# Kernel tuning notes

Measured on AMD Instinct MI355X. Metric: run time of the kernel, lower is better.

Reference implementation:

```python
import jax, jax.numpy as jnp
import numpy as np

N_NODES = 20000
N_EDGES = 640000
NODE_NF = 64
HIDDEN = 256
N_LAYERS = 4


def _linear_init(key, fan_in, fan_out, layers=None):
    shape = (fan_in, fan_out) if layers is None else (layers, fan_in, fan_out)
    scale = 1.0 / np.sqrt(fan_in)
    return jax.random.normal(key, shape, dtype=jnp.float32) * scale


def setup_inputs() -> dict:
    key = jax.random.key(0)
    ks = jax.random.split(key, 16)
    L, H = N_LAYERS, HIDDEN
    return {
        "h": jax.random.normal(ks[0], (N_NODES, NODE_NF), dtype=jnp.float32),
        "edge_index": jax.random.randint(ks[1], (2, N_EDGES), 0, N_NODES, dtype=jnp.int64),
        "coord_diff": jax.random.normal(ks[2], (N_EDGES, 3), dtype=jnp.float32),
        # embedding in / out
        "w_in": _linear_init(ks[3], NODE_NF, H),
        "b_in": jnp.zeros((H,), jnp.float32),
        "w_out": _linear_init(ks[4], H, NODE_NF),
        "b_out": jnp.zeros((NODE_NF,), jnp.float32),
        # per-layer edge MLP: Linear(2H+1 -> H), silu, Linear(H -> H), silu
        "edge_w1": _linear_init(ks[5], 2 * H + 1, H, L),
        "edge_b1": jnp.zeros((L, H), jnp.float32),
        "edge_w2": _linear_init(ks[6], H, H, L),
        "edge_b2": jnp.zeros((L, H), jnp.float32),
        # per-layer node MLP: Linear(2H -> H), silu, Linear(H -> H)
        "node_w1": _linear_init(ks[7], 2 * H, H, L),
        "node_b1": jnp.zeros((L, H), jnp.float32),
        "node_w2": _linear_init(ks[8], H, H, L),
        "node_b2": jnp.zeros((L, H), jnp.float32),
    }


def reference(h, edge_index, coord_diff, w_in, b_in, w_out, b_out,
              edge_w1, edge_b1, edge_w2, edge_b2,
              node_w1, node_b1, node_w2, node_b2):
    row, col = edge_index[0], edge_index[1]
    # radial is layer-independent: [E, 1]
    radial = jnp.sum(coord_diff ** 2, axis=1, keepdims=True)

    h = h @ w_in + b_in  # [N, H]
    n_nodes = h.shape[0]

    for l in range(N_LAYERS):
        # edge model: gather endpoints, concat with radial, 2-layer MLP
        m = jnp.concatenate([h[row], h[col], radial], axis=1)  # [E, 2H+1]
        m = jax.nn.silu(m @ edge_w1[l] + edge_b1[l])
        m = jax.nn.silu(m @ edge_w2[l] + edge_b2[l])  # [E, H]
        # node model: segment-sum aggregate over row, concat, 2-layer MLP
        agg = jax.ops.segment_sum(m, row, num_segments=n_nodes)  # [N, H]
        x = jnp.concatenate([h, agg], axis=1)  # [N, 2H]
        x = jax.nn.silu(x @ node_w1[l] + node_b1[l])
        h = x @ node_w2[l] + node_b2[l]  # recurrent=False: no residual

    return h @ w_out + b_out  # [N, node_nf]
```

## Files before the change

kernel.cpp:

```cpp
#include <hip/hip_runtime.h>
#include <hip/hip_bf16.h>
#include <cstdint>
#include <cstddef>

#define NN 20000
#define NE 640000
#define NF 64
#define HD 256
#define NL 4
#define HTS 640

typedef __attribute__((ext_vector_type(8))) short short8;
typedef __attribute__((ext_vector_type(4))) float f32x4;
typedef __attribute__((ext_vector_type(2))) float f32x2;

__device__ __forceinline__ float bf2f(unsigned short u){
  union { unsigned int i; float f; } x; x.i = ((unsigned int)u) << 16; return x.f;
}
__device__ __forceinline__ unsigned short f2bf(float f){
  union { float f; unsigned int i; } x; x.f = f;
  unsigned int r = x.i + 0x7FFFu + ((x.i >> 16) & 1u);
  return (unsigned short)(r >> 16);
}
__device__ __forceinline__ unsigned int pk2bf(float a, float b){
  union { __hip_bfloat162 h; unsigned int u; } cv;
  cv.h = __float22bfloat162_rn(float2{a, b});
  return cv.u;
}
__device__ __forceinline__ float silu_f(float v){
  float e = __builtin_amdgcn_exp2f(v * -1.442695041f);
  return v * __builtin_amdgcn_rcpf(1.0f + e);
}
__device__ __forceinline__ f32x2 silu2(f32x2 v){
  f32x2 t = v * (f32x2){-1.442695041f, -1.442695041f};
  f32x2 e = (f32x2){__builtin_amdgcn_exp2f(t.x), __builtin_amdgcn_exp2f(t.y)};
  f32x2 d = e + (f32x2){1.0f, 1.0f};
  f32x2 r = (f32x2){__builtin_amdgcn_rcpf(d.x), __builtin_amdgcn_rcpf(d.y)};
  return v * r;
}
__device__ __forceinline__ void async16(const void* g, void* l){
  __builtin_amdgcn_global_load_lds(
      (const __attribute__((address_space(1))) unsigned int*)g,
      (__attribute__((address_space(3))) unsigned int*)l, 16, 0, 0);
}

__global__ __launch_bounds__(256) void prep_small(
    const float* __restrict__ w_in, const float* __restrict__ w_out,
    const float* __restrict__ ew1, const float* __restrict__ ew2,
    const float* __restrict__ nw1, const float* __restrict__ nw2,
    const float* __restrict__ eb1,
    unsigned short* __restrict__ w_in_t, unsigned short* __restrict__ w_out_t,
    unsigned short* __restrict__ ew1cat, float* __restrict__ w1r,
    float* __restrict__ b1e,
    unsigned short* __restrict__ ew2t, unsigned short* __restrict__ nw1t,
    unsigned short* __restrict__ nw2t)
{
  const int s = blockIdx.y;
  const int tid = blockIdx.x * 256 + threadIdx.x;
  if (s == 18) {
    if (tid < NL * 512) {
      int l = tid >> 9, c = tid & 511;
      b1e[tid] = (c < 256) ? eb1[l * HD + c] : 0.0f;
    }
    return;
  }
  if (s >= 2 && s < 6) {
    int l = s - 2;
    if (tid >= 513 * HD) return;
    int k = tid / HD, n = tid - k * HD;
    float v = ew1[(size_t)l * 513 * HD + tid];
    if (k == 512) { w1r[l * HD + n] = v; return; }
    unsigned short* dst = ew1cat + (size_t)l * 512 * 256;
    if (k < 256) dst[(size_t)n * 256 + k] = f2bf(v);
    else         dst[(size_t)(256 + n) * 256 + (k - 256)] = f2bf(v);
    return;
  }
  const float* src; unsigned short* dst; int K, N;
  if (s == 0)      { src = w_in;  dst = w_in_t;  K = NF;   N = HD; }
  else if (s == 1) { src = w_out; dst = w_out_t; K = HD;   N = NF; }
  else if (s < 10) { int l = s-6;  src = ew2 + (size_t)l*HD*HD;   dst = ew2t + (size_t)l*HD*HD;  K = HD;   N = HD; }
  else if (s < 14) { int l = s-10; src = nw1 + (size_t)l*2*HD*HD; dst = nw1t + (size_t)l*HD*512; K = 2*HD; N = HD; }
  else             { int l = s-14; src = nw2 + (size_t)l*HD*HD;   dst = nw2t + (size_t)l*HD*HD;  K = HD;   N = HD; }
  if (tid >= K * N) return;
  int k = tid / N, n = tid - k * N;
  dst[(size_t)n * K + k] = f2bf(src[tid]);
}

__global__ __launch_bounds__(256) void prep_big(
    const float* __restrict__ h_in, const float* __restrict__ cd,
    unsigned short* __restrict__ hb_in, float* __restrict__ radial)
{
  const int s = blockIdx.y;
  const int tid = blockIdx.x * 256 + threadIdx.x;
  if (s == 0) {
    if (tid < NN * NF) hb_in[tid] = f2bf(h_in[tid]);
  } else {
    if (tid < NE) {
      float x = cd[tid*3+0], y = cd[tid*3+1], z = cd[tid*3+2];
      radial[tid] = x*x + y*y + z*z;
    }
  }
}

__global__ __launch_bounds__(256) void hist_k(const int* __restrict__ erow, int* __restrict__ hist){
  int e = blockIdx.x * 256 + threadIdx.x;
  if (e < NE){
    unsigned r = (unsigned)erow[e]; if (r >= NN) r = 0;
    atomicAdd(&hist[r], 1);
  }
}

__global__ __launch_bounds__(256) void scan_k(const int* __restrict__ hist,
                                              int* __restrict__ starts, int* __restrict__ cursor){
  __shared__ int part[256];
  const int t = threadIdx.x;
  const int CH = 79;
  int lo = t * CH, hi = lo + CH; if (hi > NN) hi = NN; if (lo > NN) lo = NN;
  int s = 0;
  for (int i = lo; i < hi; ++i) s += hist[i];
  part[t] = s; __syncthreads();
  for (int off = 1; off < 256; off <<= 1){
    int v = (t >= off) ? part[t - off] : 0;
    __syncthreads();
    part[t] += v;
    __syncthreads();
  }
  int base = (t == 0) ? 0 : part[t - 1];
  for (int i = lo; i < hi; ++i){ starts[i] = base; cursor[i] = base; base += hist[i]; }
  if (t == 255) starts[NN] = part[255];
}

__global__ __launch_bounds__(256) void scatter_k(const int* __restrict__ erow,
                                                 const int* __restrict__ ecol,
                                                 const float* __restrict__ radial,
                                                 int* __restrict__ cursor,
                                                 int* __restrict__ rowcol,
                                                 float* __restrict__ radial_s){
  int e = blockIdx.x * 256 + threadIdx.x;
  if (e < NE){
    unsigned r = (unsigned)erow[e]; if (r >= NN) r = 0;
    unsigned c = (unsigned)ecol[e]; if (c >= NN) c = 0;
    int pos = atomicAdd(&cursor[r], 1);
    rowcol[2*pos]   = (int)r;
    rowcol[2*pos+1] = (int)c;
    radial_s[pos] = radial[e];
  }
}

__global__ __launch_bounds__(256, 4) void node0_k(
    const unsigned short* __restrict__ hb,
    const unsigned short* __restrict__ w_in_t,
    const float* __restrict__ b_in,
    const unsigned short* __restrict__ w1cat0,
    const float* __restrict__ b1e0,
    unsigned short* __restrict__ hcur,
    unsigned short* __restrict__ hT,
    int M)
{
  __shared__ __align__(16) unsigned short As[32*64];
  __shared__ __align__(16) unsigned short Bs[256*32];
  __shared__ __align__(16) unsigned short xL[8*32*32];
  const int t = threadIdx.x;
  const int lane = t & 63, wave = t >> 6;
  const int ln15 = lane & 15, q = lane >> 4;
  const int bm = blockIdx.x;
  const int sc = (t & 3) * 8;
  const int srB = t >> 2;

  float bvin[4];
  #pragma unroll
  for (int j = 0; j < 4; ++j) bvin[j] = b_in[wave*64 + j*16 + ln15];

  f32x4 acc[2][4];
  #pragma unroll
  for (int i = 0; i < 2; ++i)
    #pragma unroll
    for (int j = 0; j < 4; ++j) acc[i][j] = (f32x4){0.f,0.f,0.f,0.f};

  async16(hb + (size_t)(bm*32 + (t >> 3)) * NF + (t & 7)*8, &As[t*8]);

  for (int kt = 0; kt < 2; ++kt) {
    #pragma unroll
    for (int i = 0; i < 4; ++i)
      async16(w_in_t + (size_t)(i*64 + srB) * NF + kt*32 + sc, &Bs[i*2048 + t*8]);
    __syncthreads();
    short8 fa[2], fb[4];
    #pragma unroll
    for (int i = 0; i < 2; ++i) fa[i] = *(const short8*)&As[(i*16 + ln15)*64 + kt*32 + q*8];
    #pragma unroll
    for (int j = 0; j < 4; ++j) fb[j] = *(const short8*)&Bs[(wave*64 + j*16 + ln15)*32 + q*8];
    #pragma unroll
    for (int i = 0; i < 2; ++i)
      #pragma unroll
      for (int j = 0; j < 4; ++j)
        acc[i][j] = __builtin_amdgcn_mfma_f32_16x16x32_bf16(fa[i], fb[j], acc[i][j], 0, 0, 0);
    __syncthreads();
  }

  #pragma unroll
  for (int i = 0; i < 2; ++i) {
    #pragma unroll
    for (int j = 0; j < 4; ++j) {
      const int n = wave*64 + j*16 + ln15;
      const int kt2 = n >> 5, k31 = n & 31;
      const int r0 = i*16 + q*4;
      const int m0 = bm*32 + r0;
      #pragma unroll
      for (int r = 0; r < 4; ++r) {
        unsigned short h = f2bf(acc[i][j][r] + bvin[j]);
        hcur[(size_t)(m0 + r) * HD + n] = h;
        xL[kt2*1024 + (r0 + r)*32 + k31] = h;
      }
    }
  }

  #pragma unroll
  for (int half = 0; half < 2; ++half) {
    #pragma unroll
    for (int i = 0; i < 2; ++i)
      #pragma unroll
      for (int j = 0; j < 4; ++j) acc[i][j] = (f32x4){0.f,0.f,0.f,0.f};
    for (int kt2 = 0; kt2 < 8; ++kt2) {
      #pragma unroll
      for (int i = 0; i < 4; ++i)
        async16(w1cat0 + (size_t)(half*256 + i*64 + srB) * 256 + kt2*32 + sc,
                &Bs[i*2048 + t*8]);
      __syncthreads();
      short8 fa[2], fb[4];
      #pragma unroll
      for (int i = 0; i < 2; ++i) fa[i] = *(const short8*)&xL[kt2*1024 + (i*16 + ln15)*32 + q*8];
      #pragma unroll
      for (int j = 0; j < 4; ++j) fb[j] = *(const short8*)&Bs[(wave*64 + j*16 + ln15)*32 + q*8];
      #pragma unroll
      for (int i = 0; i < 2; ++i)
        #pragma unroll
        for (int j = 0; j < 4; ++j)
          acc[i][j] = __builtin_amdgcn_mfma_f32_16x16x32_bf16(fa[i], fb[j], acc[i][j], 0, 0, 0);
      __syncthreads();
    }
    #pragma unroll
    for (int i = 0; i < 2; ++i) {
      #pragma unroll
      for (int j = 0; j < 4; ++j) {
        const int n = half*256 + wave*64 + j*16 + ln15;
        const float bv = b1e0[n];
        #pragma unroll
        for (int r = 0; r < 4; ++r) {
          const int m = bm*32 + i*16 + q*4 + r;
          hT[(size_t)m * HTS + n] = f2bf(acc[i][j][r] + bv);
        }
      }
    }
  }
  (void)M;
}

__global__ __launch_bounds__(256, 4) void node_k(
    unsigned short* __restrict__ hcur,
    float* __restrict__ aggF,
    const unsigned short* __restrict__ w1t,
    const float* __restrict__ b1,
    const unsigned short* __restrict__ w2t,
    const float* __restrict__ b2,
    const unsigned short* __restrict__ w1cat_next,
    const float* __restrict__ b1e_next,
    unsigned short* __restrict__ hT,
    const unsigned short* __restrict__ w_out_t,
    const float* __restrict__ b_out,
    float* __restrict__ outF,
    int M)
{
  __shared__ __align__(16) unsigned short As[32*32];
  __shared__ __align__(16) unsigned short Bs[256*32];
  __shared__ __align__(16) unsigned short xL[8*32*32];
  const int t = threadIdx.x;
  const int lane = t & 63, wave = t >> 6;
  const int ln15 = lane & 15, q = lane >> 4;
  const int bm = blockIdx.x;
  const int sc = (t & 3) * 8;
  const int srA = (t & 127) >> 2;
  const int srB = t >> 2;

  const int rowA = bm*32 + srA;
  const unsigned short* aSrc = hcur + (size_t)rowA * HD + sc;
  float* gSrc = aggF + (size_t)rowA * HD + sc;

  float bv1[4], bv2[4];
  #pragma unroll
  for (int j = 0; j < 4; ++j) {
    bv1[j] = b1[wave*64 + j*16 + ln15];
    bv2[j] = b2[wave*64 + j*16 + ln15];
  }

  f32x4 acc[2][4];
  #pragma unroll
  for (int i = 0; i < 2; ++i)
    #pragma unroll
    for (int j = 0; j < 4; ++j) acc[i][j] = (f32x4){0.f,0.f,0.f,0.f};

  for (int kt = 0; kt < 16; ++kt) {
    if (t < 128) {
      if (kt < 8) {
        async16(aSrc + kt*32, &As[t*8]);
      } else {
        float* p = gSrc + (kt-8)*32;
        float4 a0 = *(const float4*)p;
        float4 a1 = *(const float4*)(p + 4);
        union { unsigned int u[4]; short8 s8; } cv;
        cv.u[0] = pk2bf(a0.x, a0.y); cv.u[1] = pk2bf(a0.z, a0.w);
        cv.u[2] = pk2bf(a1.x, a1.y); cv.u[3] = pk2bf(a1.z, a1.w);
        *(float4*)p = float4{0.f,0.f,0.f,0.f};
        *(float4*)(p + 4) = float4{0.f,0.f,0.f,0.f};
        *(short8*)&As[t*8] = cv.s8;
      }
    }
    #pragma unroll
    for (int i = 0; i < 4; ++i)
      async16(w1t + (size_t)(i*64 + srB) * 512 + kt*32 + sc, &Bs[i*2048 + t*8]);
    __syncthreads();
    short8 fa[2], fb[4];
    #pragma unroll
    for (int i = 0; i < 2; ++i) fa[i] = *(const short8*)&As[(i*16 + ln15)*32 + q*8];
    #pragma unroll
    for (int j = 0; j < 4; ++j) fb[j] = *(const short8*)&Bs[(wave*64 + j*16 + ln15)*32 + q*8];
    #pragma unroll
    for (int i = 0; i < 2; ++i)
      #pragma unroll
      for (int j = 0; j < 4; ++j)
        acc[i][j] = __builtin_amdgcn_mfma_f32_16x16x32_bf16(fa[i], fb[j], acc[i][j], 0, 0, 0);
    __syncthreads();
  }

  #pragma unroll
  for (int i = 0; i < 2; ++i) {
    #pragma unroll
    for (int j = 0; j < 4; ++j) {
      const int k = wave*64 + j*16 + ln15;
      const int kt2 = k >> 5, k31 = k & 31;
      const f32x2 bb = (f32x2){bv1[j], bv1[j]};
      f32x2 s01 = (f32x2){acc[i][j][0], acc[i][j][1]} + bb;
      f32x2 s23 = (f32x2){acc[i][j][2], acc[i][j][3]} + bb;
      f32x2 r01 = silu2(s01);
      f32x2 r23 = silu2(s23);
      const int r0 = i*16 + q*4;
      xL[kt2*1024 + (r0  )*32 + k31] = f2bf(r01.x);
      xL[kt2*1024 + (r0+1)*32 + k31] = f2bf(r01.y);
      xL[kt2*1024 + (r0+2)*32 + k31] = f2bf(r23.x);
      xL[kt2*1024 + (r0+3)*32 + k31] = f2bf(r23.y);
    }
  }
  #pragma unroll
  for (int i = 0; i < 2; ++i)
    #pragma unroll
    for (int j = 0; j < 4; ++j) acc[i][j] = (f32x4){0.f,0.f,0.f,0.f};

  for (int kt2 = 0; kt2 < 8; ++kt2) {
    #pragma unroll
    for (int i = 0; i < 4; ++i)
      async16(w2t + (size_t)(i*64 + srB) * 256 + kt2*32 + sc, &Bs[i*2048 + t*8]);
    __syncthreads();
    short8 fa[2], fb[4];
    #pragma unroll
    for (int i = 0; i < 2; ++i) fa[i] = *(const short8*)&xL[kt2*1024 + (i*16 + ln15)*32 + q*8];
    #pragma unroll
    for (int j = 0; j < 4; ++j) fb[j] = *(const short8*)&Bs[(wave*64 + j*16 + ln15)*32 + q*8];
    #pragma unroll
    for (int i = 0; i < 2; ++i)
      #pragma unroll
      for (int j = 0; j < 4; ++j)
        acc[i][j] = __builtin_amdgcn_mfma_f32_16x16x32_bf16(fa[i], fb[j], acc[i][j], 0, 0, 0);
    __syncthreads();
  }

  #pragma unroll
  for (int i = 0; i < 2; ++i) {
    #pragma unroll
    for (int j = 0; j < 4; ++j) {
      const int n = wave*64 + j*16 + ln15;
      const int kt2 = n >> 5, k31 = n & 31;
      const int r0 = i*16 + q*4;
      const int m0 = bm*32 + r0;
      #pragma unroll
      for (int r = 0; r < 4; ++r) {
        unsigned short h = f2bf(acc[i][j][r] + bv2[j]);
        hcur[(size_t)(m0 + r) * HD + n] = h;
        xL[kt2*1024 + (r0 + r)*32 + k31] = h;
      }
    }
  }

  if (w1cat_next) {
    #pragma unroll
    for (int half = 0; half < 2; ++half) {
      #pragma unroll
      for (int i = 0; i < 2; ++i)
        #pragma unroll
        for (int j = 0; j < 4; ++j) acc[i][j] = (f32x4){0.f,0.f,0.f,0.f};
      for (int kt2 = 0; kt2 < 8; ++kt2) {
        #pragma unroll
        for (int i = 0; i < 4; ++i)
          async16(w1cat_next + (size_t)(half*256 + i*64 + srB) * 256 + kt2*32 + sc,
                  &Bs[i*2048 + t*8]);
        __syncthreads();
        short8 fa[2], fb[4];
        #pragma unroll
        for (int i = 0; i < 2; ++i) fa[i] = *(const short8*)&xL[kt2*1024 + (i*16 + ln15)*32 + q*8];
        #pragma unroll
        for (int j = 0; j < 4; ++j) fb[j] = *(const short8*)&Bs[(wave*64 + j*16 + ln15)*32 + q*8];
        #pragma unroll
        for (int i = 0; i < 2; ++i)
          #pragma unroll
          for (int j = 0; j < 4; ++j)
            acc[i][j] = __builtin_amdgcn_mfma_f32_16x16x32_bf16(fa[i], fb[j], acc[i][j], 0, 0, 0);
        __syncthreads();
      }
      #pragma unroll
      for (int i = 0; i < 2; ++i) {
        #pragma unroll
        for (int j = 0; j < 4; ++j) {
          const int n = half*256 + wave*64 + j*16 + ln15;
          const float bv = b1e_next[n];
          #pragma unroll
          for (int r = 0; r < 4; ++r) {
            const int m = bm*32 + i*16 + q*4 + r;
            hT[(size_t)m * HTS + n] = f2bf(acc[i][j][r] + bv);
          }
        }
      }
    }
  } else {
    const int nD = wave*16 + ln15;
    const float bvD = b_out[nD];
    f32x4 accD[2];
    accD[0] = (f32x4){0.f,0.f,0.f,0.f};
    accD[1] = (f32x4){0.f,0.f,0.f,0.f};
    for (int kt2 = 0; kt2 < 8; ++kt2) {
      async16(w_out_t + (size_t)srB * 256 + kt2*32 + sc, &Bs[t*8]);
      __syncthreads();
      short8 fa[2], fb;
      #pragma unroll
      for (int i = 0; i < 2; ++i) fa[i] = *(const short8*)&xL[kt2*1024 + (i*16 + ln15)*32 + q*8];
      fb = *(const short8*)&Bs[nD*32 + q*8];
      #pragma unroll
      for (int i = 0; i < 2; ++i)
        accD[i] = __builtin_amdgcn_mfma_f32_16x16x32_bf16(fa[i], fb, accD[i], 0, 0, 0);
      __syncthreads();
    }
    #pragma unroll
    for (int i = 0; i < 2; ++i) {
      #pragma unroll
      for (int r = 0; r < 4; ++r) {
        const int m = bm*32 + i*16 + q*4 + r;
        outF[(size_t)m * NF + nD] = accD[i][r] + bvD;
      }
    }
  }
  (void)M;
}

__global__ __launch_bounds__(256, 4) void edge_k(
    const unsigned short* __restrict__ hT,
    const int* __restrict__ rowcol,
    const float* __restrict__ radial_s,
    const float* __restrict__ w1r,
    const unsigned short* __restrict__ w2t,
    const float* __restrict__ b2,
    float* __restrict__ agg)
{
  __shared__ __align__(16) unsigned short MBUF[16896];
  __shared__ int   rowS[64];
  __shared__ float w1rS[256];
  unsigned short* M1  = MBUF;
  unsigned short* m2T = MBUF;

  const int t = threadIdx.x;
  const int lane = t & 63, wave = t >> 6;
  const int ln15 = lane & 15, q = lane >> 4;
  int blk = blockIdx.x;
  blk = (blk & 7) * ((int)gridDim.x >> 3) + (blk >> 3);
  const int e0 = blk * 64;
  const int sr = t >> 2;
  const int sc_swz = (((t & 3) ^ ((sr >> 1) & 3))) * 8;
  const int xq = ((q ^ ((ln15 >> 1) & 3))) * 8;

  const int2 rc = *(const int2*)(rowcol + 2*(e0 + sr));
  int rowv = 0;
  if (t < 64) rowv = rowcol[2*(e0 + t)];
  const float w1v = w1r[t];
  const float rad = radial_s[e0 + sr];

  float bv2[4];
  #pragma unroll
  for (int j = 0; j < 4; ++j) bv2[j] = b2[wave*64 + j*16 + ln15];

  const unsigned short* hr = hT + (size_t)rc.x * HTS + sc_swz;
  const unsigned short* hc = hT + (size_t)rc.y * HTS + 256 + sc_swz;

  short8 va[8], vb[8];
  #pragma unroll
  for (int ch = 0; ch < 8; ++ch) {
    va[ch] = *(const short8*)(hr + ch*32);
    vb[ch] = *(const short8*)(hc + ch*32);
  }

  if (t < 64) rowS[t] = rowv;
  w1rS[t] = w1v;

  const unsigned short* w2row[4];
  #pragma unroll
  for (int j = 0; j < 4; ++j)
    w2row[j] = w2t + (size_t)(wave*64 + j*16 + ln15) * HD + q*8;

  __syncthreads();

  const f32x2 rad2 = (f32x2){rad, rad};
  #pragma unroll
  for (int ch = 0; ch < 8; ++ch) {
    const int c0 = ch*32 + sc_swz;
    const unsigned int* ua = (const unsigned int*)&va[ch];
    const unsigned int* ub = (const unsigned int*)&vb[ch];
    union { unsigned int u[4]; short8 s; } res;
    #pragma unroll
    for (int i = 0; i < 4; ++i) {
      union { unsigned int i; float f; } alo, ahi, blo, bhi;
      alo.i = ua[i] << 16; ahi.i = ua[i] & 0xFFFF0000u;
      blo.i = ub[i] << 16; bhi.i = ub[i] & 0xFFFF0000u;
      f32x2 av = (f32x2){alo.f, ahi.f};
      f32x2 bv = (f32x2){blo.f, bhi.f};
      f32x2 wv = *(const f32x2*)&w1rS[c0 + 2*i];
      f32x2 o = av + bv;
      o = o + rad2 * wv;
      f32x2 sv = silu2(o);
      res.u[i] = pk2bf(sv.x, sv.y);
    }
    *(short8*)&M1[ch*2048 + sr*32 + (t & 3)*8] = res.s;
  }
  __syncthreads();

  f32x4 acc2[4][4];
  #pragma unroll
  for (int i = 0; i < 4; ++i)
    #pragma unroll
    for (int j = 0; j < 4; ++j) acc2[i][j] = (f32x4){0.f,0.f,0.f,0.f};

  __builtin_amdgcn_s_setprio(1);
  #pragma unroll
  for (int kt = 0; kt < 8; ++kt) {
    short8 fa[4], fb[4];
    #pragma unroll
    for (int j = 0; j < 4; ++j) fb[j] = *(const short8*)(w2row[j] + kt*32);
    #pragma unroll
    for (int i = 0; i < 4; ++i) fa[i] = *(const short8*)&M1[kt*2048 + (i*16 + ln15)*32 + xq];
    #pragma unroll
    for (int i = 0; i < 4; ++i)
      #pragma unroll
      for (int j = 0; j < 4; ++j)
        acc2[i][j] = __builtin_amdgcn_mfma_f32_16x16x32_bf16(fa[i], fb[j], acc2[i][j], 0, 0, 0);
  }
  __builtin_amdgcn_s_setprio(0);
  __syncthreads();

  #pragma unroll
  for (int i = 0; i < 4; ++i) {
    #pragma unroll
    for (int j = 0; j < 4; ++j) {
      const int n = wave*64 + j*16 + ln15;
      const f32x2 b2v = (f32x2){bv2[j], bv2[j]};
      f32x2 s01 = (f32x2){acc2[i][j][0], acc2[i][j][1]} + b2v;
      f32x2 s23 = (f32x2){acc2[i][j][2], acc2[i][j][3]} + b2v;
      f32x2 r01 = silu2(s01);
      f32x2 r23 = silu2(s23);
      const int m = i*16 + q*4;
      *(unsigned int*)&m2T[n*66 + m]     = pk2bf(r01.x, r01.y);
      *(unsigned int*)&m2T[n*66 + m + 2] = pk2bf(r23.x, r23.y);
    }
  }
  __syncthreads();

  {
    const int c = t;
    int cur = __builtin_amdgcn_readfirstlane(rowS[0]);
    float s = 0.f;
    #pragma unroll
    for (int m = 0; m < 64; m += 4) {
      unsigned int u0 = *(const unsigned int*)&m2T[c*66 + m];
      unsigned int u1 = *(const unsigned int*)&m2T[c*66 + m + 2];
      int n0 = __builtin_amdgcn_readfirstlane(rowS[m]);
      int n1 = __builtin_amdgcn_readfirstlane(rowS[m+1]);
      int n2 = __builtin_amdgcn_readfirstlane(rowS[m+2]);
      int n3 = __builtin_amdgcn_readfirstlane(rowS[m+3]);
      float f0 = bf2f((unsigned short)u0), f1 = bf2f((unsigned short)(u0 >> 16));
      float f2v = bf2f((unsigned short)u1), f3 = bf2f((unsigned short)(u1 >> 16));
      if (n0 != cur) { atomicAdd(&agg[(size_t)cur * HD + c], s); s = 0.f; cur = n0; }
      s += f0;
      if (n1 != cur) { atomicAdd(&agg[(size_t)cur * HD + c], s); s = 0.f; cur = n1; }
      s += f1;
      if (n2 != cur) { atomicAdd(&agg[(size_t)cur * HD + c], s); s = 0.f; cur = n2; }
      s += f2v;
      if (n3 != cur) { atomicAdd(&agg[(size_t)cur * HD + c], s); s = 0.f; cur = n3; }
      s += f3;
    }
    atomicAdd(&agg[(size_t)cur * HD + c], s);
  }
}

extern "C" void kernel_launch(void* const* d_in, const int* in_sizes, int n_in,
                              void* d_out, int out_size, void* d_ws, size_t ws_size,
                              hipStream_t stream)
{
  (void)in_sizes; (void)n_in; (void)out_size; (void)ws_size;
  const float* h_in  = (const float*)d_in[0];
  const int*   ei    = (const int*)d_in[1];
  const float* cd    = (const float*)d_in[2];
  const float* w_in  = (const float*)d_in[3];
  const float* b_in  = (const float*)d_in[4];
  const float* w_out = (const float*)d_in[5];
  const float* b_out = (const float*)d_in[6];
  const float* ew1   = (const float*)d_in[7];
  const float* eb1   = (const float*)d_in[8];
  const float* ew2   = (const float*)d_in[9];
  const float* eb2   = (const float*)d_in[10];
  const float* nw1   = (const float*)d_in[11];
  const float* nb1   = (const float*)d_in[12];
  const float* nw2   = (const float*)d_in[13];
  const float* nb2   = (const float*)d_in[14];
  float* out = (float*)d_out;

  char* base = (char*)d_ws;
  size_t off = 0;
  auto WS = [&](size_t bytes) -> char* {
    char* p = base + off;
    off = (off + bytes + 255) & ~(size_t)255;
    return p;
  };
  float*          radial  = (float*)WS((size_t)NE * 4);
  unsigned short* hb_in   = (unsigned short*)WS((size_t)NN * NF * 2);
  unsigned short* hcur    = (unsigned short*)WS((size_t)NN * HD * 2);
  float*          aggF    = (float*)WS((size_t)NN * HD * 4);
  unsigned short* hT      = (unsigned short*)WS((size_t)NN * HTS * 2);
  unsigned short* w_in_t  = (unsigned short*)WS((size_t)NF * HD * 2);
  unsigned short* w_out_t = (unsigned short*)WS((size_t)NF * HD * 2);
  unsigned short* ew1cat  = (unsigned short*)WS((size_t)NL * 512 * 256 * 2);
  float*          w1r     = (float*)WS((size_t)NL * HD * 4);
  float*          b1e     = (float*)WS((size_t)NL * 512 * 4);
  unsigned short* ew2t    = (unsigned short*)WS((size_t)NL * HD * HD * 2);
  unsigned short* nw1t    = (unsigned short*)WS((size_t)NL * HD * 512 * 2);
  unsigned short* nw2t    = (unsigned short*)WS((size_t)NL * HD * HD * 2);
  int*            hist    = (int*)WS((size_t)NN * 4);
  int*            starts  = (int*)WS((size_t)(NN + 1) * 4);
  int*            cursor  = (int*)WS((size_t)NN * 4);
  int*            rowcol  = (int*)WS((size_t)NE * 2 * 4);
  float*          radial_s= (float*)WS((size_t)NE * 4);

  hipMemsetAsync(hist, 0, (size_t)NN * 4, stream);
  hipMemsetAsync(aggF, 0, (size_t)NN * HD * 4, stream);
  prep_small<<<dim3(513, 19), 256, 0, stream>>>(w_in, w_out, ew1, ew2, nw1, nw2, eb1,
      w_in_t, w_out_t, ew1cat, w1r, b1e, ew2t, nw1t, nw2t);
  prep_big<<<dim3(5000, 2), 256, 0, stream>>>(h_in, cd, hb_in, radial);
  hist_k<<<NE / 256, 256, 0, stream>>>(ei, hist);
  scan_k<<<1, 256, 0, stream>>>(hist, starts, cursor);
  scatter_k<<<NE / 256, 256, 0, stream>>>(ei, ei + NE, radial, cursor, rowcol, radial_s);

  node0_k<<<NN / 32, 256, 0, stream>>>(hb_in, w_in_t, b_in, ew1cat, b1e, hcur, hT, NN);

  for (int l = 0; l < NL; ++l) {
    edge_k<<<NE / 64, 256, 0, stream>>>(hT, rowcol, radial_s,
        w1r + l * HD, ew2t + (size_t)l * HD * HD, eb2 + l * HD, aggF);
    const int last = (l == NL - 1);
    node_k<<<NN / 32, 256, 0, stream>>>(hcur, aggF,
        nw1t + (size_t)l * HD * 512, nb1 + l * HD,
        nw2t + (size_t)l * HD * HD, nb2 + l * HD,
        last ? nullptr : (ew1cat + (size_t)(l+1) * 512 * 256),
        last ? nullptr : (b1e + (size_t)(l+1) * 512),
        hT, w_out_t, b_out, out, NN);
  }
}
```

Measured before the change: 1.146 ms.

## Read node-MLP weights directly from global and parallelize CSR scan

Node kernels no longer stage weight tiles through shared memory with per-k-step barriers. They preload the whole activation tile (h and converted agg) into LDS once, then read B fragments straight from global/L2, so the inner loops run without syncthreads. The single-block serial prefix scan is replaced by a three-kernel block-parallel scan. This cuts barrier overhead and serialization, at the cost of uncoalesced, repeated global weight reads per wave.

```diff
diff --git a/kernel.cpp b/kernel.cpp
--- a/kernel.cpp
+++ b/kernel.cpp
@@ -9,6 +9,8 @@
 #define HD 256
 #define NL 4
 #define HTS 640
+#define SR 32
+#define NB 79
 
 typedef __attribute__((ext_vector_type(8))) short short8;
 typedef __attribute__((ext_vector_type(4))) float f32x4;
@@ -110,24 +112,50 @@
   }
 }
 
-__global__ __launch_bounds__(256) void scan_k(const int* __restrict__ hist,
-                                              int* __restrict__ starts, int* __restrict__ cursor){
+__global__ __launch_bounds__(256) void scan1_k(const int* __restrict__ hist, int* __restrict__ bsum){
+  __shared__ int red[256];
+  const int t = threadIdx.x;
+  const int bin = blockIdx.x * 256 + t;
+  red[t] = (bin < NN) ? hist[bin] : 0;
+  __syncthreads();
+  for (int off = 128; off > 0; off >>= 1){
+    if (t < off) red[t] += red[t + off];
+    __syncthreads();
+  }
+  if (t == 0) bsum[blockIdx.x] = red[0];
+}
+
+__global__ __launch_bounds__(256) void scan2_k(const int* __restrict__ bsum, int* __restrict__ boff){
   __shared__ int part[256];
   const int t = threadIdx.x;
-  const int CH = 79;
-  int lo = t * CH, hi = lo + CH; if (hi > NN) hi = NN; if (lo > NN) lo = NN;
-  int s = 0;
-  for (int i = lo; i < hi; ++i) s += hist[i];
-  part[t] = s; __syncthreads();
+  int v = (t < NB) ? bsum[t] : 0;
+  part[t] = v;
+  __syncthreads();
   for (int off = 1; off < 256; off <<= 1){
-    int v = (t >= off) ? part[t - off] : 0;
+    int p = (t >= off) ? part[t - off] : 0;
     __syncthreads();
-    part[t] += v;
+    part[t] += p;
     __syncthreads();
   }
-  int base = (t == 0) ? 0 : part[t - 1];
-  for (int i = lo; i < hi; ++i){ starts[i] = base; cursor[i] = base; base += hist[i]; }
-  if (t == 255) starts[NN] = part[255];
+  if (t < NB) boff[t] = part[t] - v;
+}
+
+__global__ __launch_bounds__(256) void scan3_k(const int* __restrict__ hist,
+                                               const int* __restrict__ boff,
+                                               int* __restrict__ cursor){
+  __shared__ int part[256];
+  const int t = threadIdx.x;
+  const int bin = blockIdx.x * 256 + t;
+  int v = (bin < NN) ? hist[bin] : 0;
+  part[t] = v;
+  __syncthreads();
+  for (int off = 1; off < 256; off <<= 1){
+    int p = (t >= off) ? part[t - off] : 0;
+    __syncthreads();
+    part[t] += p;
+    __syncthreads();
+  }
+  if (bin < NN) cursor[bin] = boff[blockIdx.x] + part[t] - v;
 }
 
 __global__ __launch_bounds__(256) void scatter_k(const int* __restrict__ erow,
@@ -154,47 +182,45 @@
     const unsigned short* __restrict__ w1cat0,
     const float* __restrict__ b1e0,
     unsigned short* __restrict__ hcur,
-    unsigned short* __restrict__ hT,
-    int M)
+    unsigned short* __restrict__ hT)
 {
-  __shared__ __align__(16) unsigned short As[32*64];
-  __shared__ __align__(16) unsigned short Bs[256*32];
-  __shared__ __align__(16) unsigned short xL[8*32*32];
+  __shared__ __align__(16) unsigned short LBUF[16384];
   const int t = threadIdx.x;
   const int lane = t & 63, wave = t >> 6;
   const int ln15 = lane & 15, q = lane >> 4;
   const int bm = blockIdx.x;
-  const int sc = (t & 3) * 8;
-  const int srB = t >> 2;
 
   float bvin[4];
   #pragma unroll
   for (int j = 0; j < 4; ++j) bvin[j] = b_in[wave*64 + j*16 + ln15];
 
+  {
+    const int ktb = t >> 7, rowhalf = (t >> 6) & 1, l = t & 63;
+    async16(hb + (size_t)(bm*SR + rowhalf*16 + (l >> 2)) * NF + ktb*32 + (l & 3)*8,
+            (char*)LBUF + ktb*2048 + rowhalf*1024 + l*16);
+  }
+  __syncthreads();
+
   f32x4 acc[2][4];
   #pragma unroll
   for (int i = 0; i < 2; ++i)
     #pragma unroll
     for (int j = 0; j < 4; ++j) acc[i][j] = (f32x4){0.f,0.f,0.f,0.f};
 
-  async16(hb + (size_t)(bm*32 + (t >> 3)) * NF + (t & 7)*8, &As[t*8]);
-
+  #pragma unroll
   for (int kt = 0; kt < 2; ++kt) {
-    #pragma unroll
-    for (int i = 0; i < 4; ++i)
-      async16(w_in_t + (size_t)(i*64 + srB) * NF + kt*32 + sc, &Bs[i*2048 + t*8]);
-    __syncthreads();
     short8 fa[2], fb[4];
     #pragma unroll
-    for (int i = 0; i < 2; ++i) fa[i] = *(const short8*)&As[(i*16 + ln15)*64 + kt*32 + q*8];
-    #pragma unroll
-    for (int j = 0; j < 4; ++j) fb[j] = *(const short8*)&Bs[(wave*64 + j*16 + ln15)*32 + q*8];
+    for (int i = 0; i < 2; ++i)
+      fa[i] = *(const short8*)&LBUF[kt*1024 + (i*16 + ln15)*32 + q*8];
+    #pragma unroll
+    for (int j = 0; j < 4; ++j)
+      fb[j] = *(const short8*)(w_in_t + (size_t)(wave*64 + j*16 + ln15) * NF + kt*32 + q*8);
     #pragma unroll
     for (int i = 0; i < 2; ++i)
       #pragma unroll
       for (int j = 0; j < 4; ++j)
         acc[i][j] = __builtin_amdgcn_mfma_f32_16x16x32_bf16(fa[i], fb[j], acc[i][j], 0, 0, 0);
-    __syncthreads();
   }
 
   #pragma unroll
@@ -204,15 +230,16 @@
       const int n = wave*64 + j*16 + ln15;
       const int kt2 = n >> 5, k31 = n & 31;
       const int r0 = i*16 + q*4;
-      const int m0 = bm*32 + r0;
+      const int m0 = bm*SR + r0;
       #pragma unroll
       for (int r = 0; r < 4; ++r) {
         unsigned short h = f2bf(acc[i][j][r] + bvin[j]);
         hcur[(size_t)(m0 + r) * HD + n] = h;
-        xL[kt2*1024 + (r0 + r)*32 + k31] = h;
+        LBUF[8192 + kt2*1024 + (r0 + r)*32 + k31] = h;
       }
     }
   }
+  __syncthreads();
 
   #pragma unroll
   for (int half = 0; half < 2; ++half) {
@@ -221,22 +248,18 @@
       #pragma unroll
       for (int j = 0; j < 4; ++j) acc[i][j] = (f32x4){0.f,0.f,0.f,0.f};
     for (int kt2 = 0; kt2 < 8; ++kt2) {
-      #pragma unroll
-      for (int i = 0; i < 4; ++i)
-        async16(w1cat0 + (size_t)(half*256 + i*64 + srB) * 256 + kt2*32 + sc,
-                &Bs[i*2048 + t*8]);
-      __syncthreads();
       short8 fa[2], fb[4];
       #pragma unroll
-      for (int i = 0; i < 2; ++i) fa[i] = *(const short8*)&xL[kt2*1024 + (i*16 + ln15)*32 + q*8];
-      #pragma unroll
-      for (int j = 0; j < 4; ++j) fb[j] = *(const short8*)&Bs[(wave*64 + j*16 + ln15)*32 + q*8];
+      for (int i = 0; i < 2; ++i)
+        fa[i] = *(const short8*)&LBUF[8192 + kt2*1024 + (i*16 + ln15)*32 + q*8];
+      #pragma unroll
+      for (int j = 0; j < 4; ++j)
+        fb[j] = *(const short8*)(w1cat0 + (size_t)(half*256 + wave*64 + j*16 + ln15) * 256 + kt2*32 + q*8);
       #pragma unroll
       for (int i = 0; i < 2; ++i)
         #pragma unroll
         for (int j = 0; j < 4; ++j)
           acc[i][j] = __builtin_amdgcn_mfma_f32_16x16x32_bf16(fa[i], fb[j], acc[i][j], 0, 0, 0);
-      __syncthreads();
     }
     #pragma unroll
     for (int i = 0; i < 2; ++i) {
@@ -246,13 +269,12 @@
         const float bv = b1e0[n];
         #pragma unroll
         for (int r = 0; r < 4; ++r) {
-          const int m = bm*32 + i*16 + q*4 + r;
+          const int m = bm*SR + i*16 + q*4 + r;
           hT[(size_t)m * HTS + n] = f2bf(acc[i][j][r] + bv);
         }
       }
     }
   }
-  (void)M;
 }
 
 __global__ __launch_bounds__(256, 4) void node_k(
@@ -267,23 +289,13 @@
     unsigned short* __restrict__ hT,
     const unsigned short* __restrict__ w_out_t,
     const float* __restrict__ b_out,
-    float* __restrict__ outF,
-    int M)
+    float* __restrict__ outF)
 {
-  __shared__ __align__(16) unsigned short As[32*32];
-  __shared__ __align__(16) unsigned short Bs[256*32];
-  __shared__ __align__(16) unsigned short xL[8*32*32];
+  __shared__ __align__(16) unsigned short LBUF[16384];
   const int t = threadIdx.x;
   const int lane = t & 63, wave = t >> 6;
   const int ln15 = lane & 15, q = lane >> 4;
   const int bm = blockIdx.x;
-  const int sc = (t & 3) * 8;
-  const int srA = (t & 127) >> 2;
-  const int srB = t >> 2;
-
-  const int rowA = bm*32 + srA;
-  const unsigned short* aSrc = hcur + (size_t)rowA * HD + sc;
-  float* gSrc = aggF + (size_t)rowA * HD + sc;
 
   float bv1[4], bv2[4];
   #pragma unroll
@@ -292,6 +304,39 @@
     bv2[j] = b2[wave*64 + j*16 + ln15];
   }
 
+  #pragma unroll
+  for (int s = 0; s < 4; ++s) {
+    const int hbk = s*4 + wave;
+    const int ktb = hbk >> 1, rowhalf = hbk & 1;
+    const int l = lane;
+    async16(hcur + (size_t)(bm*SR + rowhalf*16 + (l >> 2)) * HD + ktb*32 + (l & 3)*8,
+            (char*)LBUF + ktb*2048 + rowhalf*1024 + l*16);
+  }
+  {
+    const int row = t >> 3, kb = t & 7;
+    float* p = aggF + (size_t)(bm*SR + row) * HD + kb*32;
+    unsigned short* d = &LBUF[(8 + kb)*1024 + row*32];
+    #pragma unroll
+    for (int j2 = 0; j2 < 2; ++j2) {
+      float4 a0 = *(const float4*)(p + j2*16);
+      float4 a1 = *(const float4*)(p + j2*16 + 4);
+      float4 a2 = *(const float4*)(p + j2*16 + 8);
+      float4 a3 = *(const float4*)(p + j2*16 + 12);
+      union { unsigned int u[8]; short8 s8[2]; } cv;
+      cv.u[0] = pk2bf(a0.x, a0.y); cv.u[1] = pk2bf(a0.z, a0.w);
+      cv.u[2] = pk2bf(a1.x, a1.y); cv.u[3] = pk2bf(a1.z, a1.w);
+      cv.u[4] = pk2bf(a2.x, a2.y); cv.u[5] = pk2bf(a2.z, a2.w);
+      cv.u[6] = pk2bf(a3.x, a3.y); cv.u[7] = pk2bf(a3.z, a3.w);
+      *(short8*)(d + j2*16)     = cv.s8[0];
+      *(short8*)(d + j2*16 + 8) = cv.s8[1];
+      *(float4*)(p + j2*16)      = float4{0.f,0.f,0.f,0.f};
+      *(float4*)(p + j2*16 + 4)  = float4{0.f,0.f,0.f,0.f};
+      *(float4*)(p + j2*16 + 8)  = float4{0.f,0.f,0.f,0.f};
+      *(float4*)(p + j2*16 + 12) = float4{0.f,0.f,0.f,0.f};
+    }
+  }
+  __syncthreads();
+
   f32x4 acc[2][4];
   #pragma unroll
   for (int i = 0; i < 2; ++i)
@@ -299,37 +344,20 @@
     for (int j = 0; j < 4; ++j) acc[i][j] = (f32x4){0.f,0.f,0.f,0.f};
 
   for (int kt = 0; kt < 16; ++kt) {
-    if (t < 128) {
-      if (kt < 8) {
-        async16(aSrc + kt*32, &As[t*8]);
-      } else {
-        float* p = gSrc + (kt-8)*32;
-        float4 a0 = *(const float4*)p;
-        float4 a1 = *(const float4*)(p + 4);
-        union { unsigned int u[4]; short8 s8; } cv;
-        cv.u[0] = pk2bf(a0.x, a0.y); cv.u[1] = pk2bf(a0.z, a0.w);
-        cv.u[2] = pk2bf(a1.x, a1.y); cv.u[3] = pk2bf(a1.z, a1.w);
-        *(float4*)p = float4{0.f,0.f,0.f,0.f};
-        *(float4*)(p + 4) = float4{0.f,0.f,0.f,0.f};
-        *(short8*)&As[t*8] = cv.s8;
-      }
-    }
-    #pragma unroll
-    for (int i = 0; i < 4; ++i)
-      async16(w1t + (size_t)(i*64 + srB) * 512 + kt*32 + sc, &Bs[i*2048 + t*8]);
-    __syncthreads();
     short8 fa[2], fb[4];
     #pragma unroll
-    for (int i = 0; i < 2; ++i) fa[i] = *(const short8*)&As[(i*16 + ln15)*32 + q*8];
-    #pragma unroll
-    for (int j = 0; j < 4; ++j) fb[j] = *(const short8*)&Bs[(wave*64 + j*16 + ln15)*32 + q*8];
+    for (int i = 0; i < 2; ++i)
+      fa[i] = *(const short8*)&LBUF[kt*1024 + (i*16 + ln15)*32 + q*8];
+    #pragma unroll
+    for (int j = 0; j < 4; ++j)
+      fb[j] = *(const short8*)(w1t + (size_t)(wave*64 + j*16 + ln15) * 512 + kt*32 + q*8);
     #pragma unroll
     for (int i = 0; i < 2; ++i)
       #pragma unroll
       for (int j = 0; j < 4; ++j)
         acc[i][j] = __builtin_amdgcn_mfma_f32_16x16x32_bf16(fa[i], fb[j], acc[i][j], 0, 0, 0);
-    __syncthreads();
-  }
+  }
+  __syncthreads();
 
   #pragma unroll
   for (int i = 0; i < 2; ++i) {
@@ -343,33 +371,31 @@
       f32x2 r01 = silu2(s01);
       f32x2 r23 = silu2(s23);
       const int r0 = i*16 + q*4;
-      xL[kt2*1024 + (r0  )*32 + k31] = f2bf(r01.x);
-      xL[kt2*1024 + (r0+1)*32 + k31] = f2bf(r01.y);
-      xL[kt2*1024 + (r0+2)*32 + k31] = f2bf(r23.x);
-      xL[kt2*1024 + (r0+3)*32 + k31] = f2bf(r23.y);
+      LBUF[kt2*1024 + (r0  )*32 + k31] = f2bf(r01.x);
+      LBUF[kt2*1024 + (r0+1)*32 + k31] = f2bf(r01.y);
+      LBUF[kt2*1024 + (r0+2)*32 + k31] = f2bf(r23.x);
+      LBUF[kt2*1024 + (r0+3)*32 + k31] = f2bf(r23.y);
     }
   }
   #pragma unroll
   for (int i = 0; i < 2; ++i)
     #pragma unroll
     for (int j = 0; j < 4; ++j) acc[i][j] = (f32x4){0.f,0.f,0.f,0.f};
+  __syncthreads();
 
   for (int kt2 = 0; kt2 < 8; ++kt2) {
-    #pragma unroll
-    for (int i = 0; i < 4; ++i)
-      async16(w2t + (size_t)(i*64 + srB) * 256 + kt2*32 + sc, &Bs[i*2048 + t*8]);
-    __syncthreads();
     short8 fa[2], fb[4];
     #pragma unroll
-    for (int i = 0; i < 2; ++i) fa[i] = *(const short8*)&xL[kt2*1024 + (i*16 + ln15)*32 + q*8];
-    #pragma unroll
-    for (int j = 0; j < 4; ++j) fb[j] = *(const short8*)&Bs[(wave*64 + j*16 + ln15)*32 + q*8];
+    for (int i = 0; i < 2; ++i)
+      fa[i] = *(const short8*)&LBUF[kt2*1024 + (i*16 + ln15)*32 + q*8];
+    #pragma unroll
+    for (int j = 0; j < 4; ++j)
+      fb[j] = *(const short8*)(w2t + (size_t)(wave*64 + j*16 + ln15) * 256 + kt2*32 + q*8);
     #pragma unroll
     for (int i = 0; i < 2; ++i)
       #pragma unroll
       for (int j = 0; j < 4; ++j)
         acc[i][j] = __builtin_amdgcn_mfma_f32_16x16x32_bf16(fa[i], fb[j], acc[i][j], 0, 0, 0);
-    __syncthreads();
   }
 
   #pragma unroll
@@ -379,15 +405,16 @@
       const int n = wave*64 + j*16 + ln15;
       const int kt2 = n >> 5, k31 = n & 31;
       const int r0 = i*16 + q*4;
-      const int m0 = bm*32 + r0;
+      const int m0 = bm*SR + r0;
       #pragma unroll
       for (int r = 0; r < 4; ++r) {
         unsigned short h = f2bf(acc[i][j][r] + bv2[j]);
         hcur[(size_t)(m0 + r) * HD + n] = h;
-        xL[kt2*1024 + (r0 + r)*32 + k31] = h;
+        LBUF[8192 + kt2*1024 + (r0 + r)*32 + k31] = h;
       }
     }
   }
+  __syncthreads();
 
   if (w1cat_next) {
     #pragma unroll
@@ -397,22 +424,18 @@
         #pragma unroll
         for (int j = 0; j < 4; ++j) acc[i][j] = (f32x4){0.f,0.f,0.f,0.f};
       for (int kt2 = 0; kt2 < 8; ++kt2) {
-        #pragma unroll
-        for (int i = 0; i < 4; ++i)
-          async16(w1cat_next + (size_t)(half*256 + i*64 + srB) * 256 + kt2*32 + sc,
-                  &Bs[i*2048 + t*8]);
-        __syncthreads();
         short8 fa[2], fb[4];
         #pragma unroll
-        for (int i = 0; i < 2; ++i) fa[i] = *(const short8*)&xL[kt2*1024 + (i*16 + ln15)*32 + q*8];
+        for (int i = 0; i < 2; ++i)
+          fa[i] = *(const short8*)&LBUF[8192 + kt2*1024 + (i*16 + ln15)*32 + q*8];
         #pragma unroll
-        for (int j = 0; j < 4; ++j) fb[j] = *(const short8*)&Bs[(wave*64 + j*16 + ln15)*32 + q*8];
+        for (int j = 0; j < 4; ++j)
+          fb[j] = *(const short8*)(w1cat_next + (size_t)(half*256 + wave*64 + j*16 + ln15) * 256 + kt2*32 + q*8);
         #pragma unroll
         for (int i = 0; i < 2; ++i)
           #pragma unroll
           for (int j = 0; j < 4; ++j)
             acc[i][j] = __builtin_amdgcn_mfma_f32_16x16x32_bf16(fa[i], fb[j], acc[i][j], 0, 0, 0);
-        __syncthreads();
       }
       #pragma unroll
       for (int i = 0; i < 2; ++i) {
@@ -422,7 +445,7 @@
           const float bv = b1e_next[n];
           #pragma unroll
           for (int r = 0; r < 4; ++r) {
-            const int m = bm*32 + i*16 + q*4 + r;
+            const int m = bm*SR + i*16 + q*4 + r;
             hT[(size_t)m * HTS + n] = f2bf(acc[i][j][r] + bv);
           }
         }
@@ -435,27 +458,24 @@
     accD[0] = (f32x4){0.f,0.f,0.f,0.f};
     accD[1] = (f32x4){0.f,0.f,0.f,0.f};
     for (int kt2 = 0; kt2 < 8; ++kt2) {
-      async16(w_out_t + (size_t)srB * 256 + kt2*32 + sc, &Bs[t*8]);
-      __syncthreads();
-      short8 fa[2], fb;
-      #pragma unroll
-      for (int i = 0; i < 2; ++i) fa[i] = *(const short8*)&xL[kt2*1024 + (i*16 + ln15)*32 + q*8];
-      fb = *(const short8*)&Bs[nD*32 + q*8];
+      short8 fa[2];
+      #pragma unroll
+      for (int i = 0; i < 2; ++i)
+        fa[i] = *(const short8*)&LBUF[8192 + kt2*1024 + (i*16 + ln15)*32 + q*8];
+      short8 fb = *(const short8*)(w_out_t + (size_t)nD * 256 + kt2*32 + q*8);
       #pragma unroll
       for (int i = 0; i < 2; ++i)
         accD[i] = __builtin_amdgcn_mfma_f32_16x16x32_bf16(fa[i], fb, accD[i], 0, 0, 0);
-      __syncthreads();
     }
     #pragma unroll
     for (int i = 0; i < 2; ++i) {
       #pragma unroll
       for (int r = 0; r < 4; ++r) {
-        const int m = bm*32 + i*16 + q*4 + r;
+        const int m = bm*SR + i*16 + q*4 + r;
         outF[(size_t)m * NF + nD] = accD[i][r] + bvD;
       }
     }
   }
-  (void)M;
 }
 
 __global__ __launch_bounds__(256, 4) void edge_k(
@@ -647,7 +667,8 @@
   unsigned short* nw1t    = (unsigned short*)WS((size_t)NL * HD * 512 * 2);
   unsigned short* nw2t    = (unsigned short*)WS((size_t)NL * HD * HD * 2);
   int*            hist    = (int*)WS((size_t)NN * 4);
-  int*            starts  = (int*)WS((size_t)(NN + 1) * 4);
+  int*            bsum    = (int*)WS((size_t)128 * 4);
+  int*            boff    = (int*)WS((size_t)128 * 4);
   int*            cursor  = (int*)WS((size_t)NN * 4);
   int*            rowcol  = (int*)WS((size_t)NE * 2 * 4);
   float*          radial_s= (float*)WS((size_t)NE * 4);
@@ -658,20 +679,22 @@
       w_in_t, w_out_t, ew1cat, w1r, b1e, ew2t, nw1t, nw2t);
   prep_big<<<dim3(5000, 2), 256, 0, stream>>>(h_in, cd, hb_in, radial);
   hist_k<<<NE / 256, 256, 0, stream>>>(ei, hist);
-  scan_k<<<1, 256, 0, stream>>>(hist, starts, cursor);
+  scan1_k<<<NB, 256, 0, stream>>>(hist, bsum);
+  scan2_k<<<1, 256, 0, stream>>>(bsum, boff);
+  scan3_k<<<NB, 256, 0, stream>>>(hist, boff, cursor);
   scatter_k<<<NE / 256, 256, 0, stream>>>(ei, ei + NE, radial, cursor, rowcol, radial_s);
 
-  node0_k<<<NN / 32, 256, 0, stream>>>(hb_in, w_in_t, b_in, ew1cat, b1e, hcur, hT, NN);
+  node0_k<<<NN / SR, 256, 0, stream>>>(hb_in, w_in_t, b_in, ew1cat, b1e, hcur, hT);
 
   for (int l = 0; l < NL; ++l) {
     edge_k<<<NE / 64, 256, 0, stream>>>(hT, rowcol, radial_s,
         w1r + l * HD, ew2t + (size_t)l * HD * HD, eb2 + l * HD, aggF);
     const int last = (l == NL - 1);
-    node_k<<<NN / 32, 256, 0, stream>>>(hcur, aggF,
+    node_k<<<NN / SR, 256, 0, stream>>>(hcur, aggF,
         nw1t + (size_t)l * HD * 512, nb1 + l * HD,
         nw2t + (size_t)l * HD * HD, nb2 + l * HD,
         last ? nullptr : (ew1cat + (size_t)(l+1) * 512 * 256),
         last ? nullptr : (b1e + (size_t)(l+1) * 512),
-        hT, w_out_t, b_out, out, NN);
-  }
-}
+        hT, w_out_t, b_out, out);
+  }
+}
```

Result: slower. 1.246 ms (+8.7%).
